# Performance work log

Hardware: AMD Instinct MI355X
Metric: run time of the kernel (lower is better)

## Reference

```python
import jax, jax.numpy as jnp
import numpy as np
import math

D = 768
H = 12
HD = D // H  # 64


def setup_inputs() -> dict:
    key = jax.random.key(0)
    ks = jax.random.split(key, 8)
    B, S = 32, 127
    desc = jax.random.normal(ks[0], (B, S, D), dtype=jnp.float32)
    nv = jax.random.normal(ks[1], (B, S + 1, D), dtype=jnp.float32)
    def xavier(k, shape):
        fan_in, fan_out = shape[1], shape[0]
        gain = 1.0 / math.sqrt(2.0)
        limit = gain * math.sqrt(6.0 / (fan_in + fan_out))
        return jax.random.uniform(k, shape, jnp.float32, -limit, limit)
    Wq = xavier(ks[2], (D, D)); bq = jnp.zeros((D,), jnp.float32)
    Wk = xavier(ks[3], (D, D)); bk = jnp.zeros((D,), jnp.float32)
    Wv = xavier(ks[4], (D, D)); bv = jnp.zeros((D,), jnp.float32)
    # attn_proj: Linear(3*head_dim, 1)
    Wa = xavier(ks[5], (1, 3 * HD))[0]  # [3*HD]
    ba = jnp.zeros((), jnp.float32)
    return {
        "desc_embeddings": desc,
        "name_value_embeddings": nv,
        "Wq": Wq, "bq": bq, "Wk": Wk, "bk": bk, "Wv": Wv, "bv": bv,
        "Wa": Wa, "ba": ba,
    }


def _forward(desc_embeddings, name_value_embeddings, Wq, bq, Wk, bk, Wv, bv, Wa, ba):
    B, new_seq, _ = name_value_embeddings.shape
    S = new_seq - 1

    # adjacency: var-var all ones, CLS->Var row = 1, Var->CLS col = 0, CLS->CLS = 0
    adj = jnp.zeros((new_seq, new_seq), jnp.float32)
    adj = adj.at[1:, 1:].set(1.0)
    adj = adj.at[0, 1:].set(1.0)
    adj = jnp.broadcast_to(adj, (B, new_seq, new_seq))

    # q,k,v: [B, H, new_seq, HD]
    def proj(W, b):
        y = name_value_embeddings @ W.T + b
        return y.reshape(B, new_seq, H, HD).transpose(0, 2, 1, 3)
    q = proj(Wq, bq); k = proj(Wk, bk); v = proj(Wv, bv)

    # attn_proj weight split: [q_part | k_part | edge_part], each [HD]
    wq_a, wk_a, we_a = Wa[:HD], Wa[HD:2 * HD], Wa[2 * HD:]

    # q/k scalar contributions per (b,h,i) and (b,h,j)
    lq = jnp.einsum('bhid,d->bhi', q, wq_a)  # [B,H,new_seq]
    lk = jnp.einsum('bhjd,d->bhj', k, wk_a)  # [B,H,new_seq]

    # edge_attr[b,i,j] per head h (head slice of concat[node_i_desc, node_j_desc]):
    # edge vector = concat(desc_i, desc_j)[h*HD:(h+1)*HD] viewed as [H, HD] of 2D dims.
    # concat(desc_i, desc_j) has 2D dims -> reshaped to [H, HD] means head h takes
    # slice [h*HD:(h+1)*HD] of the 2D-dim concat. Heads 0..H/2-1 come from desc_i,
    # heads H/2..H-1 come from desc_j. Compute edge dot with we_a accordingly.
    # desc_full[b,t] : [B,S,D]. Build per-head contributions:
    # for h < H//2: edge slice = desc_i[h*HD:(h+1)*HD]  -> depends only on i
    # for h >= H//2: edge slice = desc_j[(h-H//2)*HD:(h-H//2+1)*HD] -> depends only on j
    desc_heads = desc_embeddings.reshape(B, S, H // 2, 2 * HD)  # wrong split; do directly
    # Direct: per head h, slice indices into the 2D concat vector
    dh = desc_embeddings.reshape(B, S, H, HD)  # desc split into H chunks of HD (covers D = H*HD)
    # concat(desc_i,desc_j) reshaped to [H,HD]: heads 0..H/2-1 use dh_i[:, :, h],
    # heads H/2..H-1 use dh_j[:, :, h - H/2]
    e_dot = jnp.einsum('bshd,d->bsh', dh, jnp.broadcast_to(we_a, (HD,)))  # placeholder, recompute per head below
    # per-head edge scalar contribution for var-var edges:
    ei = jnp.einsum('bshd,d->bhs', dh, we_a)  # contribution if head slice comes from desc at position s
    Hh = H // 2
    # var-var logits edge part: for h<Hh depends on i; for h>=Hh depends on j
    le_i = ei[:, :Hh, :]   # [B,Hh,S] depends on i (row)
    le_j = ei[:, Hh:, :]   # [B,Hh,S] depends on j (col)

    # CLS edges: cls_edge_attr = concat(desc, desc) at position t (the var index)
    # row 0 (CLS->var j): edge = concat(desc_j, desc_j) -> head h slice:
    #   h<Hh: dh_j[h]; h>=Hh: dh_j[h-Hh]  -> scalar ei[b,h,j] with h mapped
    e_cls = jnp.concatenate([ei[:, :Hh, :], ei[:, :Hh, :]], axis=1) * 0  # init
    e_cls = jnp.concatenate([le_i, le_i], axis=1)  # [B,H,S]: head h<Hh uses dh[h], h>=Hh uses dh[h-Hh]
    # note ei[:, :Hh] corresponds to dh chunks 0..Hh-1 ; for h>=Hh slice is dh[h-Hh] -> same le_i

    # Assemble full logits [B,H,new_seq,new_seq]
    logits = lq[:, :, :, None] + lk[:, :, None, :]
    # edge contributions (only where adj==1; edge_attr zeroed elsewhere by mask mult)
    edge = jnp.zeros((B, H, new_seq, new_seq), jnp.float32)
    # var-var block [1:,1:]
    ev = jnp.zeros((B, H, S, S), jnp.float32)
    ev = ev + jnp.pad(le_i, ((0, 0), (0, Hh), (0, 0)))[:, :, :, None] * 0  # keep shapes
    ev_i = jnp.concatenate([le_i, jnp.zeros_like(le_j)], axis=1)  # h<Hh: i-dependent
    ev_j = jnp.concatenate([jnp.zeros_like(le_i), le_j], axis=1)  # h>=Hh: j-dependent
    ev = ev_i[:, :, :, None] + ev_j[:, :, None, :]  # [B,H,S,S]
    edge = edge.at[:, :, 1:, 1:].set(ev)
    # CLS row (0, 1:): cls_edge = concat(desc_j,desc_j); j = column var
    edge = edge.at[:, :, 0, 1:].set(e_cls)
    # CLS col (1:, 0): cls_edge = concat(desc_i,desc_i) BUT adj[:,1:,0]=0 so edge_attr
    # multiplied by adj -> zero; also masked out. edge stays 0, but torch zeroes it too.
    # mask edge by adjacency (edge_attr *= adj)
    edge = edge * adj[:, None, :, :]
    logits = logits + edge + ba

    mask = (adj[:, None, :, :] == 0).astype(jnp.float32) * -1e9
    logits = logits + mask
    attn = jax.nn.softmax(logits, axis=-1)  # [B,H,new_seq,new_seq]
    ctx = jnp.einsum('bhij,bhjd->bhid', attn, v)
    basis_outputs = ctx.transpose(0, 2, 1, 3)  # [B,new_seq,H,HD]
    return basis_outputs, attn


def reference(desc_embeddings, name_value_embeddings, Wq, bq, Wk, bk, Wv, bv, Wa, ba):
    return _forward(desc_embeddings, name_value_embeddings, Wq, bq, Wk, bk, Wv, bv, Wa, ba)
```

## Files before the change

### kernel.cpp

```cpp
#include <hip/hip_runtime.h>

#define NB 32
#define NS 128
#define SD 127
#define ND 768
#define NH 12
#define HD 64

__device__ inline float wredSum(float v){
  #pragma unroll
  for (int off=32; off>0; off>>=1) v += __shfl_xor(v, off);
  return v;
}
__device__ inline float wredMax(float v){
  #pragma unroll
  for (int off=32; off>0; off>>=1) v = fmaxf(v, __shfl_xor(v, off));
  return v;
}

__global__ __launch_bounds__(256)
void fold_k(const float* __restrict__ Wk, const float* __restrict__ bk,
            const float* __restrict__ Wa, float* __restrict__ uk,
            float* __restrict__ bkdot){
  int blk = blockIdx.x;
  int h = blk/12, cb = blk%12;
  int t = threadIdx.x;
  int c0 = t & 63, dg = t >> 6;
  const float* base = Wk + (size_t)(h*HD + dg*16)*ND + cb*64 + c0;
  float acc = 0.f;
  #pragma unroll
  for (int i=0;i<16;++i) acc += base[(size_t)i*ND] * Wa[64 + dg*16 + i];
  __shared__ float red[4][64];
  red[dg][c0] = acc;
  __syncthreads();
  if (dg==0) uk[h*ND + cb*64 + c0] = red[0][c0]+red[1][c0]+red[2][c0]+red[3][c0];
  if (blk==0 && t < NH){
    float a = 0.f;
    for (int d=0; d<64; ++d) a += bk[t*HD+d]*Wa[64+d];
    bkdot[t] = a;
  }
}

__global__ __launch_bounds__(256)
void lk_ei_init(const float* __restrict__ nv, const float* __restrict__ desc,
                const float* __restrict__ uk, const float* __restrict__ bkdot,
                const float* __restrict__ Wa, const float* __restrict__ bv,
                float* __restrict__ lk, float* __restrict__ ei,
                float* __restrict__ ctx){
  __shared__ float sh[ND];
  int blk = blockIdx.x;
  int wave = threadIdx.x >> 6, lane = threadIdx.x & 63;
  if (blk < NB*NS){
    int b = blk >> 7, j = blk & 127;
    const float* row = nv + (size_t)blk * ND;
    for (int c = threadIdx.x; c < ND; c += 256) sh[c] = row[c];
    __syncthreads();
    #pragma unroll
    for (int hh=0; hh<3; ++hh){
      int h = wave*3 + hh;
      float acc = 0.f;
      #pragma unroll
      for (int k=0; k<12; ++k) acc += sh[lane+64*k]*uk[h*ND + lane+64*k];
      acc = wredSum(acc);
      if (lane==0) lk[(b*NH + h)*NS + j] = acc + bkdot[h];
    }
  } else if (blk < NB*NS + NB*SD){
    int bs = blk - NB*NS;
    int b = bs / SD, s = bs % SD;
    float wea = Wa[128 + lane];
    const float* row = desc + (size_t)bs * ND;
    #pragma unroll
    for (int hh=0; hh<3; ++hh){
      int h = wave + hh*4;
      float v = row[h*HD + lane] * wea;
      v = wredSum(v);
      if (lane==0) ei[(b*NH + h)*NS + s] = v;
    }
  } else {
    int idx = (blk - (NB*NS + NB*SD))*256 + threadIdx.x;
    int dq = idx & 15;
    int r  = (idx >> 4) % 24;
    int h  = r >> 1;
    const float* bb = bv + h*HD + dq*4;
    float4 v = { bb[0], bb[1], bb[2], bb[3] };
    ((float4*)ctx)[idx] = v;
  }
}

__global__ __launch_bounds__(256)
void wm_proj(const float* __restrict__ nv, const float* __restrict__ lk,
             const float* __restrict__ ei, const float* __restrict__ Wv,
             float* __restrict__ ctx, float* __restrict__ out){
  int blk = blockIdx.x;
  int cc = blk % 3, bh = blk / 3;
  int b = bh / NH, h = bh % NH;
  __shared__ float w0[NS], w1[NS], m0[256], m1[256];
  int t = threadIdx.x, wave = t >> 6, lane = t & 63;

  if (wave < 2){
    const float* lkrow = lk + bh*NS;
    const float* eirow = ei + (b*NH + (wave==0 ? (h%6) : h))*NS;
    float g = (wave==0) ? 1.f : (h>=6 ? 1.f : 0.f);
    float x0 = (lane>=1) ? lkrow[lane] + g*eirow[lane-1] : -3.0e38f;
    float x1 = lkrow[lane+64] + g*eirow[lane+63];
    float mm = wredMax(fmaxf(x0,x1));
    float e0 = (lane>=1) ? __expf(x0-mm) : 0.f;
    float e1 = __expf(x1-mm);
    float s  = wredSum(e0+e1);
    float inv = 1.f/s;
    float* wd = wave ? w1 : w0;
    wd[lane]    = e0*inv;
    wd[lane+64] = e1*inv;
  }
  __syncthreads();

  {
    float4* ao = (float4*)(out + (size_t)NB*NS*ND + (size_t)bh*NS*NS);
    int nrows = (NS - cc + 2)/3;
    for (int idx=t; idx<nrows*32; idx+=256){
      int rr = idx>>5, q = idx&31;
      int r = cc + 3*rr;
      const float* src = (r==0) ? w0 : w1;
      float4 v = { src[q*4], src[q*4+1], src[q*4+2], src[q*4+3] };
      ao[r*32+q] = v;
    }
  }

  const float* nvp = nv + (size_t)(b*NS)*ND + cc*256 + t;
  float a0 = 0.f, a1 = 0.f;
  #pragma unroll 4
  for (int j=1; j<NS; ++j){
    float x = nvp[(size_t)j*ND];
    a0 += w0[j]*x;
    a1 += w1[j]*x;
  }
  m0[t] = a0; m1[t] = a1;
  __syncthreads();

  const float* wvbase = Wv + (size_t)(h*HD)*ND + cc*256;
  #pragma unroll 4
  for (int dd=0; dd<16; ++dd){
    int d = wave*16 + dd;
    const float* wvr = wvbase + (size_t)d*ND;
    float p0 = 0.f, p1 = 0.f;
    #pragma unroll
    for (int k=0; k<4; ++k){
      float wv = wvr[lane + 64*k];
      p0 += wv*m0[lane + 64*k];
      p1 += wv*m1[lane + 64*k];
    }
    p0 = wredSum(p0); p1 = wredSum(p1);
    if (lane==0){
      atomicAdd(&ctx[((size_t)b*24 + h*2    )*HD + d], p0);
      atomicAdd(&ctx[((size_t)b*24 + h*2 + 1)*HD + d], p1);
    }
  }
}

__global__ __launch_bounds__(256)
void basis_kernel(const float* __restrict__ ctx, float* __restrict__ out){
  int idx = blockIdx.x*256 + threadIdx.x;
  int dq = idx & 15;
  int h  = (idx >> 4) % NH;
  int i  = (idx / 192) & 127;
  int b  = idx / 24576;
  ((float4*)out)[idx] = ((const float4*)ctx)[((b*NH + h)*2 + (i != 0))*16 + dq];
}

extern "C" void kernel_launch(void* const* d_in, const int* in_sizes, int n_in,
                              void* d_out, int out_size, void* d_ws, size_t ws_size,
                              hipStream_t stream) {
  const float* desc = (const float*)d_in[0];
  const float* nv   = (const float*)d_in[1];
  const float* Wk   = (const float*)d_in[4];
  const float* bk   = (const float*)d_in[5];
  const float* Wv   = (const float*)d_in[6];
  const float* bv   = (const float*)d_in[7];
  const float* Wa   = (const float*)d_in[8];
  float* out = (float*)d_out;
  float* ws  = (float*)d_ws;

  float* uk    = ws;
  float* bkdot = ws + 9216;
  float* ei    = ws + 9232;
  float* lkbuf = ws + 58384;
  float* ctx   = ws + 107536;

  fold_k      <<<144,  256, 0, stream>>>(Wk, bk, Wa, uk, bkdot);
  lk_ei_init  <<<8208, 256, 0, stream>>>(nv, desc, uk, bkdot, Wa, bv, lkbuf, ei, ctx);
  wm_proj     <<<1152, 256, 0, stream>>>(nv, lkbuf, ei, Wv, ctx, out);
  basis_kernel<<<3072, 256, 0, stream>>>(ctx, out);
}
```

Measured before the change: 150.8 us.

## Split weighted-sum pipeline: separate softmax, batched nv reduction, fused projection and output write

```diff
diff --git a/kernel.cpp b/kernel.cpp
--- a/kernel.cpp
+++ b/kernel.cpp
@@ -42,11 +42,10 @@
 }
 
 __global__ __launch_bounds__(256)
-void lk_ei_init(const float* __restrict__ nv, const float* __restrict__ desc,
-                const float* __restrict__ uk, const float* __restrict__ bkdot,
-                const float* __restrict__ Wa, const float* __restrict__ bv,
-                float* __restrict__ lk, float* __restrict__ ei,
-                float* __restrict__ ctx){
+void lk_ei(const float* __restrict__ nv, const float* __restrict__ desc,
+           const float* __restrict__ uk, const float* __restrict__ bkdot,
+           const float* __restrict__ Wa,
+           float* __restrict__ lk, float* __restrict__ ei){
   __shared__ float sh[ND];
   int blk = blockIdx.x;
   int wave = threadIdx.x >> 6, lane = threadIdx.x & 63;
@@ -64,7 +63,7 @@
       acc = wredSum(acc);
       if (lane==0) lk[(b*NH + h)*NS + j] = acc + bkdot[h];
     }
-  } else if (blk < NB*NS + NB*SD){
+  } else {
     int bs = blk - NB*NS;
     int b = bs / SD, s = bs % SD;
     float wea = Wa[128 + lane];
@@ -76,95 +75,113 @@
       v = wredSum(v);
       if (lane==0) ei[(b*NH + h)*NS + s] = v;
     }
-  } else {
-    int idx = (blk - (NB*NS + NB*SD))*256 + threadIdx.x;
-    int dq = idx & 15;
-    int r  = (idx >> 4) % 24;
-    int h  = r >> 1;
-    const float* bb = bv + h*HD + dq*4;
-    float4 v = { bb[0], bb[1], bb[2], bb[3] };
-    ((float4*)ctx)[idx] = v;
+  }
+}
+
+__global__ __launch_bounds__(128)
+void softmax_k(const float* __restrict__ lk, const float* __restrict__ ei,
+               float* __restrict__ w, float* __restrict__ wT){
+  int bh = blockIdx.x;
+  int b = bh / NH, h = bh % NH;
+  int t = threadIdx.x, wave = t >> 6, lane = t & 63;
+  const float* lkrow = lk + bh*NS;
+  const float* eirow = ei + (b*NH + (wave==0 ? (h%6) : h))*NS;
+  float g = (wave==0) ? 1.f : (h>=6 ? 1.f : 0.f);
+  float x0 = (lane>=1) ? lkrow[lane] + g*eirow[lane-1] : -3.0e38f;
+  float x1 = lkrow[lane+64] + g*eirow[lane+63];
+  float mm = wredMax(fmaxf(x0,x1));
+  float e0 = (lane>=1) ? __expf(x0-mm) : 0.f;
+  float e1 = __expf(x1-mm);
+  float s  = wredSum(e0+e1);
+  float inv = 1.f/s;
+  float v0 = e0*inv, v1 = e1*inv;
+  w[(bh*2+wave)*NS + lane]      = v0;
+  w[(bh*2+wave)*NS + lane+64]   = v1;
+  int r = h*2 + wave;
+  wT[(b*NS + lane)*24 + r]      = v0;
+  wT[(b*NS + lane+64)*24 + r]   = v1;
+}
+
+__global__ __launch_bounds__(192)
+void m_kernel(const float* __restrict__ nv, const float* __restrict__ wT,
+              float* __restrict__ m_part){
+  int blk = blockIdx.x;
+  int b = blk >> 2, jg = blk & 3;
+  int t = threadIdx.x;
+  __shared__ float wld[32][24];
+  for (int i=t; i<32*24; i+=192) ((float*)wld)[i] = wT[(size_t)(b*NS + jg*32)*24 + i];
+  __syncthreads();
+  const float4* nvb = (const float4*)(nv + ((size_t)b*NS + jg*32)*ND);
+  float4 acc[24];
+  #pragma unroll
+  for (int r=0; r<24; ++r) acc[r] = make_float4(0.f,0.f,0.f,0.f);
+  #pragma unroll 2
+  for (int jj=0; jj<32; ++jj){
+    float4 x = nvb[jj*192 + t];
+    #pragma unroll
+    for (int r=0; r<24; ++r){
+      float wr = wld[jj][r];
+      acc[r].x += wr*x.x; acc[r].y += wr*x.y;
+      acc[r].z += wr*x.z; acc[r].w += wr*x.w;
+    }
+  }
+  #pragma unroll
+  for (int r=0; r<24; ++r){
+    ((float4*)(m_part + ((size_t)(b*24 + r)*4 + jg)*ND))[t] = acc[r];
   }
 }
 
 __global__ __launch_bounds__(256)
-void wm_proj(const float* __restrict__ nv, const float* __restrict__ lk,
-             const float* __restrict__ ei, const float* __restrict__ Wv,
-             float* __restrict__ ctx, float* __restrict__ out){
-  int blk = blockIdx.x;
-  int cc = blk % 3, bh = blk / 3;
+void proj_write(const float* __restrict__ m_part, const float* __restrict__ Wv,
+                const float* __restrict__ bv, const float* __restrict__ w,
+                float* __restrict__ out){
+  int bh = blockIdx.x;
   int b = bh / NH, h = bh % NH;
-  __shared__ float w0[NS], w1[NS], m0[256], m1[256];
   int t = threadIdx.x, wave = t >> 6, lane = t & 63;
-
-  if (wave < 2){
-    const float* lkrow = lk + bh*NS;
-    const float* eirow = ei + (b*NH + (wave==0 ? (h%6) : h))*NS;
-    float g = (wave==0) ? 1.f : (h>=6 ? 1.f : 0.f);
-    float x0 = (lane>=1) ? lkrow[lane] + g*eirow[lane-1] : -3.0e38f;
-    float x1 = lkrow[lane+64] + g*eirow[lane+63];
-    float mm = wredMax(fmaxf(x0,x1));
-    float e0 = (lane>=1) ? __expf(x0-mm) : 0.f;
-    float e1 = __expf(x1-mm);
-    float s  = wredSum(e0+e1);
-    float inv = 1.f/s;
-    float* wd = wave ? w1 : w0;
-    wd[lane]    = e0*inv;
-    wd[lane+64] = e1*inv;
-  }
-  __syncthreads();
-
-  {
-    float4* ao = (float4*)(out + (size_t)NB*NS*ND + (size_t)bh*NS*NS);
-    int nrows = (NS - cc + 2)/3;
-    for (int idx=t; idx<nrows*32; idx+=256){
-      int rr = idx>>5, q = idx&31;
-      int r = cc + 3*rr;
-      const float* src = (r==0) ? w0 : w1;
-      float4 v = { src[q*4], src[q*4+1], src[q*4+2], src[q*4+3] };
-      ao[r*32+q] = v;
-    }
-  }
-
-  const float* nvp = nv + (size_t)(b*NS)*ND + cc*256 + t;
-  float a0 = 0.f, a1 = 0.f;
-  #pragma unroll 4
-  for (int j=1; j<NS; ++j){
-    float x = nvp[(size_t)j*ND];
-    a0 += w0[j]*x;
-    a1 += w1[j]*x;
-  }
-  m0[t] = a0; m1[t] = a1;
-  __syncthreads();
-
-  const float* wvbase = Wv + (size_t)(h*HD)*ND + cc*256;
+  __shared__ float msum[2][ND];
+  __shared__ float wrow[2][NS];
+  __shared__ float cvec[2][HD];
+  wrow[t>>7][t&127] = w[(size_t)bh*2*NS + t];
+  for (int i=t; i<2*ND; i+=256){
+    int rl = (i >= ND);
+    int c  = i - rl*ND;
+    const float* mp = m_part + ((size_t)(b*24 + h*2 + rl)*4)*ND + c;
+    msum[rl][c] = mp[0] + mp[ND] + mp[2*ND] + mp[3*ND];
+  }
+  __syncthreads();
   #pragma unroll 4
   for (int dd=0; dd<16; ++dd){
     int d = wave*16 + dd;
-    const float* wvr = wvbase + (size_t)d*ND;
-    float p0 = 0.f, p1 = 0.f;
-    #pragma unroll
-    for (int k=0; k<4; ++k){
+    const float* wvr = Wv + (size_t)(h*HD + d)*ND;
+    float p0=0.f, p1=0.f;
+    #pragma unroll
+    for (int k=0; k<12; ++k){
       float wv = wvr[lane + 64*k];
-      p0 += wv*m0[lane + 64*k];
-      p1 += wv*m1[lane + 64*k];
+      p0 += wv*msum[0][lane + 64*k];
+      p1 += wv*msum[1][lane + 64*k];
     }
     p0 = wredSum(p0); p1 = wredSum(p1);
     if (lane==0){
-      atomicAdd(&ctx[((size_t)b*24 + h*2    )*HD + d], p0);
-      atomicAdd(&ctx[((size_t)b*24 + h*2 + 1)*HD + d], p1);
-    }
-  }
-}
-
-__global__ __launch_bounds__(256)
-void basis_kernel(const float* __restrict__ ctx, float* __restrict__ out){
-  int idx = blockIdx.x*256 + threadIdx.x;
-  int dq = idx & 15;
-  int h  = (idx >> 4) % NH;
-  int i  = (idx / 192) & 127;
-  int b  = idx / 24576;
-  ((float4*)out)[idx] = ((const float4*)ctx)[((b*NH + h)*2 + (i != 0))*16 + dq];
+      float bb = bv[h*HD + d];
+      cvec[0][d] = p0 + bb;
+      cvec[1][d] = p1 + bb;
+    }
+  }
+  __syncthreads();
+  float4* ao = (float4*)(out + (size_t)NB*NS*ND + (size_t)bh*NS*NS);
+  for (int idx=t; idx<4096; idx+=256){
+    int i = idx>>5, q = idx&31;
+    const float* src = (i==0) ? wrow[0] : wrow[1];
+    float4 v = { src[q*4], src[q*4+1], src[q*4+2], src[q*4+3] };
+    ao[idx] = v;
+  }
+  float* bo = out + (size_t)b*NS*ND + h*HD;
+  for (int idx=t; idx<2048; idx+=256){
+    int i = idx>>4, q = idx&15;
+    const float* src = (i==0) ? cvec[0] : cvec[1];
+    float4 v = { src[q*4], src[q*4+1], src[q*4+2], src[q*4+3] };
+    *(float4*)(bo + (size_t)i*ND + q*4) = v;
+  }
 }
 
 extern "C" void kernel_launch(void* const* d_in, const int* in_sizes, int n_in,
@@ -180,14 +197,17 @@
   float* out = (float*)d_out;
   float* ws  = (float*)d_ws;
 
-  float* uk    = ws;
-  float* bkdot = ws + 9216;
-  float* ei    = ws + 9232;
-  float* lkbuf = ws + 58384;
-  float* ctx   = ws + 107536;
-
-  fold_k      <<<144,  256, 0, stream>>>(Wk, bk, Wa, uk, bkdot);
-  lk_ei_init  <<<8208, 256, 0, stream>>>(nv, desc, uk, bkdot, Wa, bv, lkbuf, ei, ctx);
-  wm_proj     <<<1152, 256, 0, stream>>>(nv, lkbuf, ei, Wv, ctx, out);
-  basis_kernel<<<3072, 256, 0, stream>>>(ctx, out);
-}
+  float* uk     = ws;
+  float* bkdot  = ws + 9216;
+  float* ei     = ws + 9232;
+  float* lkbuf  = ws + 58384;
+  float* wbuf   = ws + 107536;
+  float* wT     = ws + 205840;
+  float* m_part = ws + 304144;
+
+  fold_k    <<<144,  256, 0, stream>>>(Wk, bk, Wa, uk, bkdot);
+  lk_ei     <<<8160, 256, 0, stream>>>(nv, desc, uk, bkdot, Wa, lkbuf, ei);
+  softmax_k <<<384,  128, 0, stream>>>(lkbuf, ei, wbuf, wT);
+  m_kernel  <<<128,  192, 0, stream>>>(nv, wT, m_part);
+  proj_write<<<384,  256, 0, stream>>>(m_part, Wv, bv, wbuf, out);
+}
```

New measurement: 143.0 us. 1.05x faster.
